# Performance work log

Measured on AMD Instinct MI355X. Metric: run time of the kernel, lower is better.

The kernel has to match this reference:

```python
import jax, jax.numpy as jnp
import numpy as np

B, C, H, W = 16, 128, 128, 128
NUM_HEADS, HEAD_DIM = 4, 32
HIDDEN = NUM_HEADS * HEAD_DIM  # 128
GROUPS = 32
EPS = 1e-5


def setup_inputs() -> dict:
    key = jax.random.key(0)
    ks = jax.random.split(key, 6)
    # conv1x1 weights: torch Conv2d weight (out, in, 1, 1) -> stored as (out, in)
    fan_qkv = C
    fan_proj = HIDDEN
    return {
        "x": jax.random.normal(ks[0], (B, C, H, W), dtype=jnp.float32),
        "gn_w": jnp.ones((C,), dtype=jnp.float32),
        "gn_b": jnp.zeros((C,), dtype=jnp.float32),
        "qkv_w": jax.random.normal(ks[1], (3 * HIDDEN, C), dtype=jnp.float32) / np.sqrt(fan_qkv),
        "proj_w": jax.random.normal(ks[2], (C, HIDDEN), dtype=jnp.float32) / np.sqrt(fan_proj),
        "proj_b": jax.random.normal(ks[3], (C,), dtype=jnp.float32) * 0.01,
    }


def reference(x, gn_w, gn_b, qkv_w, proj_w, proj_b):
    b, c, h, w = x.shape
    n = h * w
    residual = x
    # GroupNorm(32 groups), biased variance, affine
    xg = x.reshape(b, GROUPS, c // GROUPS, h, w)
    mu = xg.mean(axis=(2, 3, 4), keepdims=True)
    var = xg.var(axis=(2, 3, 4), keepdims=True)
    xn = ((xg - mu) * jax.lax.rsqrt(var + EPS)).reshape(b, c, h, w)
    xn = xn * gn_w[None, :, None, None] + gn_b[None, :, None, None]
    # 1x1 conv QKV (no bias); channel layout -> (b, 3, heads, head_dim, n)
    qkv = jnp.einsum('oc,bchw->bohw', qkv_w, xn)
    qkv = qkv.reshape(b, 3, NUM_HEADS, HEAD_DIM, n)
    q, k, v = qkv[:, 0], qkv[:, 1], qkv[:, 2]
    q = jax.nn.softmax(q, axis=-1)   # over spatial positions
    k = jax.nn.softmax(k, axis=-2)   # over head_dim
    # context = k @ v^T : (b,h,D,D)
    ctx = jnp.einsum('bhdn,bhen->bhde', k, v)
    # out = context^T @ q : (b,h,D,n)
    out = jnp.einsum('bhde,bhdn->bhen', ctx, q)
    out = out.reshape(b, HIDDEN, h, w)
    # 1x1 conv projection (with bias)
    out = jnp.einsum('co,bohw->bchw', proj_w, out) + proj_b[None, :, None, None]
    return out + residual
```

## Files before the change

### kernel.cpp

```cpp
#include <hip/hip_runtime.h>


#define B_ 16
#define C_ 128
#define N_ 16384

typedef short bf16x8 __attribute__((ext_vector_type(8)));
typedef float f32x4 __attribute__((ext_vector_type(4)));
typedef unsigned u32x2 __attribute__((ext_vector_type(2)));

__device__ __forceinline__ ushort f2bf(float f) {
    union { float f; unsigned u; } v; v.f = f;
    unsigned r = (v.u + 0x7FFFu + ((v.u >> 16) & 1u)) >> 16;
    return (ushort)r;
}
__device__ __forceinline__ float bf2f(unsigned h) {
    union { unsigned u; float f; } v; v.u = h << 16;
    return v.f;
}

__global__ void k_stats(const float* __restrict__ x, const float* __restrict__ gnw,
                        const float* __restrict__ gnb, float* __restrict__ sc,
                        float* __restrict__ bi,
                        const float* __restrict__ qkvw, ushort* __restrict__ wbf) {
    int bg = blockIdx.x;
    if (bg >= 512) {
        int i = (bg - 512) * 1024 + threadIdx.x;
        if (i < 384 * 128) wbf[i] = f2bf(qkvw[i]);
        return;
    }
    const float4* p = (const float4*)(x + (size_t)bg * (4 * N_));
    float s = 0.f, s2 = 0.f;
    for (int i = threadIdx.x; i < N_; i += 1024) {
        float4 v = p[i];
        s  += v.x + v.y + v.z + v.w;
        s2 += v.x * v.x + v.y * v.y + v.z * v.z + v.w * v.w;
    }
    #pragma unroll
    for (int d = 32; d > 0; d >>= 1) { s += __shfl_xor(s, d); s2 += __shfl_xor(s2, d); }
    __shared__ float ls[16], ls2[16];
    int wid = threadIdx.x >> 6, lane = threadIdx.x & 63;
    if (lane == 0) { ls[wid] = s; ls2[wid] = s2; }
    __syncthreads();
    if (threadIdx.x == 0) {
        float S = 0.f, S2 = 0.f;
        #pragma unroll
        for (int i = 0; i < 16; ++i) { S += ls[i]; S2 += ls2[i]; }
        float m = S / 65536.f;
        float var = S2 / 65536.f - m * m;
        float rs = rsqrtf(var + 1e-5f);
        int b = bg >> 5, g = bg & 31;
        #pragma unroll
        for (int i = 0; i < 4; ++i) {
            int c = g * 4 + i;
            float scv = rs * gnw[c];
            sc[b * 128 + c] = scv;
            bi[b * 128 + c] = gnb[c] - m * scv;
        }
    }
}

#define MFMA16(A, Bv, Cc) __builtin_amdgcn_mfma_f32_16x16x32_bf16(A, Bv, Cc, 0, 0, 0)

#define DO_Q(J) do { \
    f32x4 acc = {0.f, 0.f, 0.f, 0.f}; \
    acc = MFMA16(wf[J][0], xb[0], acc); acc = MFMA16(wf[J][1], xb[1], acc); \
    acc = MFMA16(wf[J][2], xb[2], acc); acc = MFMA16(wf[J][3], xb[3], acc); \
    qacc[J][0] += __expf(acc[0]); qacc[J][1] += __expf(acc[1]); \
    qacc[J][2] += __expf(acc[2]); qacc[J][3] += __expf(acc[3]); \
} while (0)

#define DO_K(JLO, H) do { \
    f32x4 aL = {0.f, 0.f, 0.f, 0.f}, aH = {0.f, 0.f, 0.f, 0.f}; \
    aL = MFMA16(wf[JLO][0], xb[0], aL);     aH = MFMA16(wf[(JLO)+1][0], xb[0], aH); \
    aL = MFMA16(wf[JLO][1], xb[1], aL);     aH = MFMA16(wf[(JLO)+1][1], xb[1], aH); \
    aL = MFMA16(wf[JLO][2], xb[2], aL);     aH = MFMA16(wf[(JLO)+1][2], xb[2], aH); \
    aL = MFMA16(wf[JLO][3], xb[3], aL);     aH = MFMA16(wf[(JLO)+1][3], xb[3], aH); \
    float eL0 = __expf(aL[0]), eL1 = __expf(aL[1]), eL2 = __expf(aL[2]), eL3 = __expf(aL[3]); \
    float eH0 = __expf(aH[0]), eH1 = __expf(aH[1]), eH2 = __expf(aH[2]), eH3 = __expf(aH[3]); \
    float s = eL0 + eL1 + eL2 + eL3 + eH0 + eH1 + eH2 + eH3; \
    s += __shfl_xor(s, 16); s += __shfl_xor(s, 32); \
    float rinv = 1.f / s; \
    ksm[H][lg * 4 + 0][nloc] = f2bf(eL0 * rinv); \
    ksm[H][lg * 4 + 1][nloc] = f2bf(eL1 * rinv); \
    ksm[H][lg * 4 + 2][nloc] = f2bf(eL2 * rinv); \
    ksm[H][lg * 4 + 3][nloc] = f2bf(eL3 * rinv); \
    ksm[H][16 + lg * 4 + 0][nloc] = f2bf(eH0 * rinv); \
    ksm[H][16 + lg * 4 + 1][nloc] = f2bf(eH1 * rinv); \
    ksm[H][16 + lg * 4 + 2][nloc] = f2bf(eH2 * rinv); \
    ksm[H][16 + lg * 4 + 3][nloc] = f2bf(eH3 * rinv); \
} while (0)

#define DO_V(J, HV, EB) do { \
    f32x4 acc = {0.f, 0.f, 0.f, 0.f}; \
    acc = MFMA16(wf[J][0], xb[0], acc); acc = MFMA16(wf[J][1], xb[1], acc); \
    acc = MFMA16(wf[J][2], xb[2], acc); acc = MFMA16(wf[J][3], xb[3], acc); \
    vls[HV][(EB) + lg * 4 + 0][nloc] = f2bf(acc[0]); \
    vls[HV][(EB) + lg * 4 + 1][nloc] = f2bf(acc[1]); \
    vls[HV][(EB) + lg * 4 + 2][nloc] = f2bf(acc[2]); \
    vls[HV][(EB) + lg * 4 + 3][nloc] = f2bf(acc[3]); \
} while (0)

__global__ __launch_bounds__(256, 2) void k_main(
    const float* __restrict__ x, const ushort* __restrict__ wbf,
    const float* __restrict__ scA, const float* __restrict__ biA,
    float* __restrict__ qsumP, float* __restrict__ ctxP) {
    int blk = blockIdx.x;
    int b = blk >> 6, nb = blk & 63;
    int tid = threadIdx.x, wid = tid >> 6, lane = tid & 63;
    int l15 = lane & 15, lg = lane >> 4;

    __shared__ __align__(16) ushort xs[4096];
    __shared__ __align__(16) ushort ksm[4][32][40];
    __shared__ __align__(16) ushort vls[4][32][40];

    bf16x8 wf[6][4];
    {
        const ushort* wr = wbf + (size_t)(wid * 96 + l15) * 128 + lg * 8;
        #pragma unroll
        for (int j = 0; j < 6; ++j)
            #pragma unroll
            for (int kc = 0; kc < 4; ++kc)
                wf[j][kc] = *(const bf16x8*)(wr + j * 2048 + kc * 32);
    }

    float qacc[6][4];
    #pragma unroll
    for (int j = 0; j < 6; ++j)
        #pragma unroll
        for (int r = 0; r < 4; ++r) qacc[j][r] = 0.f;
    f32x4 cacc[2][2];
    #pragma unroll
    for (int di = 0; di < 2; ++di)
        #pragma unroll
        for (int ei = 0; ei < 2; ++ei) cacc[di][ei] = (f32x4){0.f, 0.f, 0.f, 0.f};

    const int pk_ = tid & 7, pcb = tid >> 3;
    const float* xrow = x + (size_t)b * (C_ * N_) + nb * 256 + pk_ * 4;
    float scv[4], biv[4];
    #pragma unroll
    for (int i = 0; i < 4; ++i) {
        scv[i] = scA[b * 128 + pcb * 4 + i];
        biv[i] = biA[b * 128 + pcb * 4 + i];
    }
    unsigned boffj[4];
    #pragma unroll
    for (int j = 0; j < 4; ++j) {
        int n = pk_ * 4 + j;
        boffj[j] = (unsigned)(n * 256 + (((pcb >> 1) * 16) ^ ((n & 7) << 4)) + (pcb & 1) * 8);
    }

    float4 vbuf[4];
    #pragma unroll
    for (int i = 0; i < 4; ++i)
        vbuf[i] = *(const float4*)(xrow + (size_t)(pcb * 4 + i) * N_);

    for (int ch = 0; ch < 8; ++ch) {
        __syncthreads();
        unsigned e[4][4];
        #pragma unroll
        for (int i = 0; i < 4; ++i) {
            float s = scv[i], t = biv[i];
            e[i][0] = f2bf(vbuf[i].x * s + t);
            e[i][1] = f2bf(vbuf[i].y * s + t);
            e[i][2] = f2bf(vbuf[i].z * s + t);
            e[i][3] = f2bf(vbuf[i].w * s + t);
        }
        if (ch < 7) {
            #pragma unroll
            for (int i = 0; i < 4; ++i)
                vbuf[i] = *(const float4*)(xrow + (size_t)(pcb * 4 + i) * N_ + (ch + 1) * 32);
        }
        #pragma unroll
        for (int j = 0; j < 4; ++j) {
            u32x2 wj;
            wj.x = e[0][j] | (e[1][j] << 16);
            wj.y = e[2][j] | (e[3][j] << 16);
            *(u32x2*)((char*)xs + boffj[j]) = wj;
        }
        __syncthreads();

        #pragma unroll
        for (int nt = 0; nt < 2; ++nt) {
            int row = nt * 16 + l15;
            bf16x8 xb[4];
            #pragma unroll
            for (int kc = 0; kc < 4; ++kc) {
                unsigned off = (unsigned)(row * 256 +
                    (((kc * 4 + lg) * 16) ^ ((row & 7) << 4)));
                xb[kc] = *(const bf16x8*)((const char*)xs + off);
            }
            int nloc = nt * 16 + l15;

            if (wid == 0) {
                DO_Q(0); DO_Q(1); DO_Q(2); DO_Q(3); DO_Q(4); DO_Q(5);
            } else if (wid == 1) {
                DO_Q(0); DO_Q(1); DO_K(2, 0); DO_K(4, 1);
            } else if (wid == 2) {
                DO_K(0, 2); DO_K(2, 3); DO_V(4, 0, 0); DO_V(5, 0, 16);
            } else {
                DO_V(0, 1, 0); DO_V(1, 1, 16); DO_V(2, 2, 0);
                DO_V(3, 2, 16); DO_V(4, 3, 0); DO_V(5, 3, 16);
            }
        }
        __syncthreads();

        {
            bf16x8 A0 = *(const bf16x8*)&ksm[wid][l15][lg * 8];
            bf16x8 A1 = *(const bf16x8*)&ksm[wid][16 + l15][lg * 8];
            bf16x8 B0 = *(const bf16x8*)&vls[wid][l15][lg * 8];
            bf16x8 B1 = *(const bf16x8*)&vls[wid][16 + l15][lg * 8];
            cacc[0][0] = MFMA16(A0, B0, cacc[0][0]);
            cacc[0][1] = MFMA16(A0, B1, cacc[0][1]);
            cacc[1][0] = MFMA16(A1, B0, cacc[1][0]);
            cacc[1][1] = MFMA16(A1, B1, cacc[1][1]);
        }
    }

    int nq = (wid == 0) ? 6 : (wid == 1 ? 2 : 0);
    #pragma unroll
    for (int j = 0; j < 6; ++j) {
        if (j < nq) {
            #pragma unroll
            for (int r = 0; r < 4; ++r) {
                float s = qacc[j][r];
                s += __shfl_xor(s, 1); s += __shfl_xor(s, 2);
                s += __shfl_xor(s, 4); s += __shfl_xor(s, 8);
                if (l15 == 0)
                    qsumP[(size_t)blk * 128 + (wid * 6 + j) * 16 + lg * 4 + r] = s;
            }
        }
    }
    float* cp = ctxP + (size_t)blk * 4096 + wid * 1024;
    #pragma unroll
    for (int di = 0; di < 2; ++di)
        #pragma unroll
        for (int ei = 0; ei < 2; ++ei)
            #pragma unroll
            for (int r = 0; r < 4; ++r)
                cp[(di * 16 + lg * 4 + r) * 32 + ei * 16 + l15] = cacc[di][ei][r];
}

__global__ void k_red(float* __restrict__ ctxP) {
    int blk = blockIdx.x;
    int b = blk >> 3, sl = blk & 7;
    float* base = ctxP + (size_t)b * 64 * 4096;
    #pragma unroll
    for (int r = 0; r < 2; ++r) {
        int i = sl * 512 + r * 256 + threadIdx.x;
        float s = 0.f;
        for (int q = 0; q < 64; ++q) s += base[(size_t)q * 4096 + i];
        base[i] = s;
    }
}

__global__ void k_comb(const float* __restrict__ ctxP, const float* __restrict__ qsumP,
                       const float* __restrict__ projw, ushort* __restrict__ mpp) {
    int b = blockIdx.x, tid = threadIdx.x;
    __shared__ float ctx[4096];
    __shared__ float qinv[128];
    for (int i = tid; i < 4096; i += 256)
        ctx[i] = ctxP[(size_t)b * 64 * 4096 + i];
    if (tid < 128) {
        float s = 0.f;
        const float* p = qsumP + (size_t)b * 64 * 128 + tid;
        for (int q = 0; q < 64; ++q) s += p[q * 128];
        qinv[tid] = 1.f / s;
    }
    __syncthreads();
    int c = tid >> 1, hd0 = (tid & 1) * 64;
    unsigned ow[32];
    for (int k = 0; k < 64; ++k) {
        int hd = hd0 + k, h = hd >> 5, d = hd & 31;
        const float* pw = projw + c * 128 + h * 32;
        const float* cx = ctx + h * 1024 + d * 32;
        float s = 0.f;
        #pragma unroll 8
        for (int e = 0; e < 32; ++e) s += pw[e] * cx[e];
        s *= qinv[hd];
        ushort bv = f2bf(s);
        if (k & 1) ow[k >> 1] |= ((unsigned)bv) << 16; else ow[k >> 1] = bv;
    }
    ushort* dst = mpp + ((size_t)(b * 128 + c)) * 128 + hd0;
    #pragma unroll
    for (int q = 0; q < 8; ++q) {
        uint4 t; t.x = ow[q * 4]; t.y = ow[q * 4 + 1]; t.z = ow[q * 4 + 2]; t.w = ow[q * 4 + 3];
        ((uint4*)dst)[q] = t;
    }
}

#define ATT_STRIDE 136
__global__ __launch_bounds__(256) void k_final(
    const ushort* __restrict__ wbf, const ushort* __restrict__ mpp,
    const float* __restrict__ scA, const float* __restrict__ biA,
    const float* __restrict__ projb, const float* __restrict__ x,
    float* __restrict__ out) {
    int blk = blockIdx.x;
    int b = blk >> 8, nb = blk & 255;
    int tid = threadIdx.x, wid = tid >> 6, lane = tid & 63;
    int l15 = lane & 15, lg = lane >> 4;
    int n0 = nb * 64;

    __shared__ __align__(16) char lds[33792];
    ushort* xs   = (ushort*)lds;
    char*   att  = lds;
    ushort* eqls = (ushort*)(lds + 17408);

    bf16x8 wq[2][4];
    #pragma unroll
    for (int j = 0; j < 2; ++j) {
        const ushort* wr = wbf + (size_t)((wid * 2 + j) * 16 + l15) * 128 + lg * 8;
        #pragma unroll
        for (int kc = 0; kc < 4; ++kc) wq[j][kc] = *(const bf16x8*)(wr + kc * 32);
    }
    bf16x8 bm[2][4];
    #pragma unroll
    for (int ctk = 0; ctk < 2; ++ctk) {
        const ushort* br = mpp + ((size_t)(b * 128 + (wid * 2 + ctk) * 16 + l15)) * 128 + lg * 8;
        #pragma unroll
        for (int kc = 0; kc < 4; ++kc) bm[ctk][kc] = *(const bf16x8*)(br + kc * 32);
    }

    const int pk_ = tid & 15, pcb = tid >> 4;
    float4 xv[8];
    {
        const float* xrow = x + (size_t)b * (C_ * N_) + n0 + pk_ * 4;
        unsigned e[8][4];
        #pragma unroll
        for (int i = 0; i < 8; ++i) {
            int c = pcb * 8 + i;
            float s = scA[b * 128 + c], t = biA[b * 128 + c];
            xv[i] = *(const float4*)(xrow + (size_t)c * N_);
            e[i][0] = f2bf(xv[i].x * s + t);
            e[i][1] = f2bf(xv[i].y * s + t);
            e[i][2] = f2bf(xv[i].z * s + t);
            e[i][3] = f2bf(xv[i].w * s + t);
        }
        #pragma unroll
        for (int j = 0; j < 4; ++j) {
            int n = pk_ * 4 + j;
            uint4 wj;
            wj.x = e[0][j] | (e[1][j] << 16);
            wj.y = e[2][j] | (e[3][j] << 16);
            wj.z = e[4][j] | (e[5][j] << 16);
            wj.w = e[6][j] | (e[7][j] << 16);
            unsigned byte = (unsigned)(n * 256 + ((pcb * 16) ^ ((n & 7) << 4)));
            *(uint4*)((char*)xs + byte) = wj;
        }
    }
    __syncthreads();

    #pragma unroll
    for (int nt = 0; nt < 4; ++nt) {
        int row = nt * 16 + l15;
        bf16x8 xb[4];
        #pragma unroll
        for (int kc = 0; kc < 4; ++kc) {
            unsigned off = (unsigned)(row * 256 + (((kc * 4 + lg) * 16) ^ ((row & 7) << 4)));
            xb[kc] = *(const bf16x8*)((const char*)xs + off);
        }
        #pragma unroll
        for (int j = 0; j < 2; ++j) {
            f32x4 a = {0.f, 0.f, 0.f, 0.f};
            #pragma unroll
            for (int kc = 0; kc < 4; ++kc) a = MFMA16(wq[j][kc], xb[kc], a);
            u32x2 pk;
            pk.x = (unsigned)f2bf(__expf(a[0])) | ((unsigned)f2bf(__expf(a[1])) << 16);
            pk.y = (unsigned)f2bf(__expf(a[2])) | ((unsigned)f2bf(__expf(a[3])) << 16);
            int ot = wid * 2 + j;
            unsigned byte = (unsigned)(row * 256 +
                (((ot * 2 + (lg >> 1)) * 16) ^ ((row & 7) << 4)) + (lg & 1) * 8);
            *(u32x2*)((char*)eqls + byte) = pk;
        }
    }
    __syncthreads();

    #pragma unroll
    for (int nt = 0; nt < 4; ++nt) {
        int row = nt * 16 + l15;
        bf16x8 af[4];
        #pragma unroll
        for (int kc = 0; kc < 4; ++kc) {
            unsigned off = (unsigned)(row * 256 + (((kc * 4 + lg) * 16) ^ ((row & 7) << 4)));
            af[kc] = *(const bf16x8*)((const char*)eqls + off);
        }
        #pragma unroll
        for (int ctk = 0; ctk < 2; ++ctk) {
            f32x4 a = {0.f, 0.f, 0.f, 0.f};
            #pragma unroll
            for (int kc = 0; kc < 4; ++kc) a = MFMA16(af[kc], bm[ctk][kc], a);
            int c = (wid * 2 + ctk) * 16 + l15;
            u32x2 pk;
            pk.x = (unsigned)f2bf(a[0]) | ((unsigned)f2bf(a[1]) << 16);
            pk.y = (unsigned)f2bf(a[2]) | ((unsigned)f2bf(a[3]) << 16);
            unsigned byte = (unsigned)(c * ATT_STRIDE +
                (((nt * 2 + (lg >> 1)) * 16) ^ ((c & 7) << 4)) + (lg & 1) * 8);
            *(u32x2*)(att + byte) = pk;
        }
    }
    __syncthreads();

    {
        size_t obase = (size_t)b * (C_ * N_) + n0 + pk_ * 4;
        #pragma unroll
        for (int i = 0; i < 8; ++i) {
            int c = pcb * 8 + i;
            unsigned byte = (unsigned)(c * ATT_STRIDE +
                (((pk_ >> 1) * 16) ^ ((c & 7) << 4)) + (pk_ & 1) * 8);
            u32x2 pk = *(const u32x2*)(att + byte);
            float pbv = projb[c];
            f32x4 o4;
            o4[0] = bf2f(pk.x & 0xffffu) + pbv + xv[i].x;
            o4[1] = bf2f(pk.x >> 16)     + pbv + xv[i].y;
            o4[2] = bf2f(pk.y & 0xffffu) + pbv + xv[i].z;
            o4[3] = bf2f(pk.y >> 16)     + pbv + xv[i].w;
            *(f32x4*)(out + obase + (size_t)c * N_) = o4;
        }
    }
}

extern "C" void kernel_launch(void* const* d_in, const int* in_sizes, int n_in,
                              void* d_out, int out_size, void* d_ws, size_t ws_size,
                              hipStream_t stream) {
    const float* x     = (const float*)d_in[0];
    const float* gnw   = (const float*)d_in[1];
    const float* gnb   = (const float*)d_in[2];
    const float* qkvw  = (const float*)d_in[3];
    const float* projw = (const float*)d_in[4];
    const float* projb = (const float*)d_in[5];
    float* out = (float*)d_out;

    char* ws = (char*)d_ws;
    ushort* wbf   = (ushort*)(ws);
    float*  qsumP = (float*)(ws + 102400);
    ushort* mpp   = (ushort*)(ws + 626688);
    float*  sc    = (float*)(ws + 1150976);
    float*  bi    = (float*)(ws + 1159168);
    float*  ctxP  = (float*)(ws + 1167360);

    k_stats<<<560,  1024, 0, stream>>>(x, gnw, gnb, sc, bi, qkvw, wbf);
    k_main <<<1024, 256,  0, stream>>>(x, wbf, sc, bi, qsumP, ctxP);
    k_red  <<<128,  256,  0, stream>>>(ctxP);
    k_comb <<<16,   256,  0, stream>>>(ctxP, qsumP, projw, mpp);
    k_final<<<4096, 256,  0, stream>>>(wbf, mpp, sc, bi, projb, x, out);
}
```

Before: 204.4 us.

## Fuse context reduction and projection combine into k_main via last-block atomic counter

```diff
diff --git a/kernel.cpp b/kernel.cpp
--- a/kernel.cpp
+++ b/kernel.cpp
@@ -22,9 +22,11 @@
 __global__ void k_stats(const float* __restrict__ x, const float* __restrict__ gnw,
                         const float* __restrict__ gnb, float* __restrict__ sc,
                         float* __restrict__ bi,
-                        const float* __restrict__ qkvw, ushort* __restrict__ wbf) {
+                        const float* __restrict__ qkvw, ushort* __restrict__ wbf,
+                        unsigned* __restrict__ cnt) {
     int bg = blockIdx.x;
     if (bg >= 512) {
+        if (bg == 512 && threadIdx.x < 16) cnt[threadIdx.x] = 0u;
         int i = (bg - 512) * 1024 + threadIdx.x;
         if (i < 384 * 128) wbf[i] = f2bf(qkvw[i]);
         return;
@@ -104,15 +106,19 @@
 __global__ __launch_bounds__(256, 2) void k_main(
     const float* __restrict__ x, const ushort* __restrict__ wbf,
     const float* __restrict__ scA, const float* __restrict__ biA,
-    float* __restrict__ qsumP, float* __restrict__ ctxP) {
+    float* __restrict__ qsumP, float* __restrict__ ctxP,
+    const float* __restrict__ projw, ushort* __restrict__ mpp,
+    unsigned* __restrict__ cnt) {
     int blk = blockIdx.x;
     int b = blk >> 6, nb = blk & 63;
     int tid = threadIdx.x, wid = tid >> 6, lane = tid & 63;
     int l15 = lane & 15, lg = lane >> 4;
 
-    __shared__ __align__(16) ushort xs[4096];
-    __shared__ __align__(16) ushort ksm[4][32][40];
-    __shared__ __align__(16) ushort vls[4][32][40];
+    __shared__ __align__(16) char smem[28672];
+    __shared__ unsigned lastFlag;
+    ushort* xs = (ushort*)smem;
+    ushort (*ksm)[32][40] = (ushort(*)[32][40])(smem + 8192);
+    ushort (*vls)[32][40] = (ushort(*)[32][40])(smem + 18432);
 
     bf16x8 wf[6][4];
     {
@@ -239,53 +245,48 @@
             #pragma unroll
             for (int r = 0; r < 4; ++r)
                 cp[(di * 16 + lg * 4 + r) * 32 + ei * 16 + l15] = cacc[di][ei][r];
-}
-
-__global__ void k_red(float* __restrict__ ctxP) {
-    int blk = blockIdx.x;
-    int b = blk >> 3, sl = blk & 7;
-    float* base = ctxP + (size_t)b * 64 * 4096;
-    #pragma unroll
-    for (int r = 0; r < 2; ++r) {
-        int i = sl * 512 + r * 256 + threadIdx.x;
-        float s = 0.f;
-        for (int q = 0; q < 64; ++q) s += base[(size_t)q * 4096 + i];
-        base[i] = s;
-    }
-}
-
-__global__ void k_comb(const float* __restrict__ ctxP, const float* __restrict__ qsumP,
-                       const float* __restrict__ projw, ushort* __restrict__ mpp) {
-    int b = blockIdx.x, tid = threadIdx.x;
-    __shared__ float ctx[4096];
-    __shared__ float qinv[128];
-    for (int i = tid; i < 4096; i += 256)
-        ctx[i] = ctxP[(size_t)b * 64 * 4096 + i];
-    if (tid < 128) {
-        float s = 0.f;
-        const float* p = qsumP + (size_t)b * 64 * 128 + tid;
-        for (int q = 0; q < 64; ++q) s += p[q * 128];
-        qinv[tid] = 1.f / s;
-    }
-    __syncthreads();
-    int c = tid >> 1, hd0 = (tid & 1) * 64;
-    unsigned ow[32];
-    for (int k = 0; k < 64; ++k) {
-        int hd = hd0 + k, h = hd >> 5, d = hd & 31;
-        const float* pw = projw + c * 128 + h * 32;
-        const float* cx = ctx + h * 1024 + d * 32;
-        float s = 0.f;
-        #pragma unroll 8
-        for (int e = 0; e < 32; ++e) s += pw[e] * cx[e];
-        s *= qinv[hd];
-        ushort bv = f2bf(s);
-        if (k & 1) ow[k >> 1] |= ((unsigned)bv) << 16; else ow[k >> 1] = bv;
-    }
-    ushort* dst = mpp + ((size_t)(b * 128 + c)) * 128 + hd0;
-    #pragma unroll
-    for (int q = 0; q < 8; ++q) {
-        uint4 t; t.x = ow[q * 4]; t.y = ow[q * 4 + 1]; t.z = ow[q * 4 + 2]; t.w = ow[q * 4 + 3];
-        ((uint4*)dst)[q] = t;
+
+    __threadfence();
+    __syncthreads();
+    if (tid == 0) lastFlag = atomicAdd(cnt + b, 1u);
+    __syncthreads();
+    if (lastFlag == 63u) {
+        __threadfence();
+        float* ctx = (float*)smem;
+        float* qinv = (float*)(smem + 16384);
+        for (int i = tid; i < 4096; i += 256) {
+            float s = 0.f;
+            const float* p = ctxP + (size_t)b * 64 * 4096 + i;
+            for (int q = 0; q < 64; ++q) s += p[(size_t)q * 4096];
+            ctx[i] = s;
+        }
+        if (tid < 128) {
+            float s = 0.f;
+            const float* p = qsumP + (size_t)b * 64 * 128 + tid;
+            for (int q = 0; q < 64; ++q) s += p[q * 128];
+            qinv[tid] = 1.f / s;
+        }
+        __syncthreads();
+        int c = tid >> 1, hd0 = (tid & 1) * 64;
+        ushort* dst = mpp + ((size_t)(b * 128 + c)) * 128 + hd0;
+        for (int q8 = 0; q8 < 8; ++q8) {
+            unsigned ow[4];
+            #pragma unroll
+            for (int kk = 0; kk < 8; ++kk) {
+                int k = q8 * 8 + kk;
+                int hd = hd0 + k, h = hd >> 5, d = hd & 31;
+                const float* pw = projw + c * 128 + h * 32;
+                const float* cx = ctx + h * 1024 + d * 32;
+                float s = 0.f;
+                #pragma unroll 8
+                for (int e = 0; e < 32; ++e) s += pw[e] * cx[e];
+                s *= qinv[hd];
+                ushort bv = f2bf(s);
+                if (kk & 1) ow[kk >> 1] |= ((unsigned)bv) << 16; else ow[kk >> 1] = bv;
+            }
+            uint4 t; t.x = ow[0]; t.y = ow[1]; t.z = ow[2]; t.w = ow[3];
+            ((uint4*)dst)[q8] = t;
+        }
     }
 }
 
@@ -431,16 +432,15 @@
     float* out = (float*)d_out;
 
     char* ws = (char*)d_ws;
-    ushort* wbf   = (ushort*)(ws);
-    float*  qsumP = (float*)(ws + 102400);
-    ushort* mpp   = (ushort*)(ws + 626688);
-    float*  sc    = (float*)(ws + 1150976);
-    float*  bi    = (float*)(ws + 1159168);
-    float*  ctxP  = (float*)(ws + 1167360);
-
-    k_stats<<<560,  1024, 0, stream>>>(x, gnw, gnb, sc, bi, qkvw, wbf);
-    k_main <<<1024, 256,  0, stream>>>(x, wbf, sc, bi, qsumP, ctxP);
-    k_red  <<<128,  256,  0, stream>>>(ctxP);
-    k_comb <<<16,   256,  0, stream>>>(ctxP, qsumP, projw, mpp);
+    ushort*   wbf   = (ushort*)(ws);
+    unsigned* cnt   = (unsigned*)(ws + 100352);
+    float*    qsumP = (float*)(ws + 102400);
+    ushort*   mpp   = (ushort*)(ws + 626688);
+    float*    sc    = (float*)(ws + 1150976);
+    float*    bi    = (float*)(ws + 1159168);
+    float*    ctxP  = (float*)(ws + 1167360);
+
+    k_stats<<<560,  1024, 0, stream>>>(x, gnw, gnb, sc, bi, qkvw, wbf, cnt);
+    k_main <<<1024, 256,  0, stream>>>(x, wbf, sc, bi, qsumP, ctxP, projw, mpp, cnt);
     k_final<<<4096, 256,  0, stream>>>(wbf, mpp, sc, bi, projb, x, out);
 }
```

Result: slower. 409.5 us (+100.4%).
